# Kernel optimization log

Measured on AMD Instinct MI355X. Metric: run time of the kernel, lower is better.

The kernel has to match this reference:

```python
import jax, jax.numpy as jnp
import numpy as np

N_NODES = 10000
N_EDGES = 160000
NUM_FEAT = 14
DIM = 256


def gat_conv(x, src, dst, W, a_s, a_d, b, concat):
    """PyG GATConv: W [H*C, F_in], a_s/a_d [H, C], edges src->dst (self-loops included)."""
    H, C = a_s.shape
    N = x.shape[0]
    h = (x @ W.T).reshape(N, H, C)                       # [N,H,C]
    alpha_src = (h * a_s).sum(-1)                        # [N,H]
    alpha_dst = (h * a_d).sum(-1)                        # [N,H]
    e = jax.nn.leaky_relu(alpha_src[src] + alpha_dst[dst], negative_slope=0.2)  # [E,H]
    emax = jax.ops.segment_max(e, dst, num_segments=N)   # [N,H]
    emax = jnp.where(jnp.isneginf(emax), 0.0, emax)
    ex = jnp.exp(e - emax[dst])
    denom = jax.ops.segment_sum(ex, dst, num_segments=N)
    coef = ex / (denom[dst] + 1e-16)                     # segment softmax over in-edges
    out = jax.ops.segment_sum(h[src] * coef[..., None], dst, num_segments=N)  # [N,H,C]
    out = out.reshape(N, H * C) if concat else out.mean(axis=1)
    return out + b


def setup_inputs() -> dict:
    key = jax.random.key(0)
    ks = jax.random.split(key, 24)
    d = DIM
    f = NUM_FEAT
    def w(k, shape, fan_in):
        return jax.random.normal(k, shape, dtype=jnp.float32) * (1.0 / np.sqrt(fan_in))
    inp = {
        "x": jax.random.normal(ks[0], (N_NODES, f), dtype=jnp.float32),
        "edge_index": jax.random.randint(ks[1], (2, N_EDGES), 0, N_NODES, dtype=jnp.int64
                                         if jax.config.jax_enable_x64 else jnp.int32),
        # conv1: 14 -> 4 heads x 256
        "W1": w(ks[2], (4 * d, f), f),
        "a1s": w(ks[3], (4, d), d), "a1d": w(ks[4], (4, d), d),
        "b1": jnp.zeros((4 * d,), jnp.float32),
        "lw1": w(ks[5], (4 * d, f), f), "lb1": jnp.zeros((4 * d,), jnp.float32),
        # conv2: 1024 -> 4 heads x 256
        "W2": w(ks[6], (4 * d, 4 * d), 4 * d),
        "a2s": w(ks[7], (4, d), d), "a2d": w(ks[8], (4, d), d),
        "b2": jnp.zeros((4 * d,), jnp.float32),
        "lw2": w(ks[9], (4 * d, 4 * d), 4 * d), "lb2": jnp.zeros((4 * d,), jnp.float32),
        # conv3: 1024 -> 6 heads x 256, mean over heads
        "W3": w(ks[10], (6 * d, 4 * d), 4 * d),
        "a3s": w(ks[11], (6, d), d), "a3d": w(ks[12], (6, d), d),
        "b3": jnp.zeros((d,), jnp.float32),
        "lw3": w(ks[13], (d, 4 * d), 4 * d), "lb3": jnp.zeros((d,), jnp.float32),
    }
    return inp


def reference(x, edge_index, W1, a1s, a1d, b1, lw1, lb1,
              W2, a2s, a2d, b2, lw2, lb2,
              W3, a3s, a3d, b3, lw3, lb3):
    N = x.shape[0]
    loops = jnp.arange(N, dtype=edge_index.dtype)
    src = jnp.concatenate([edge_index[0], loops])
    dst = jnp.concatenate([edge_index[1], loops])
    x1 = jax.nn.elu(gat_conv(x, src, dst, W1, a1s, a1d, b1, True) + x @ lw1.T + lb1)
    x2 = jax.nn.elu(gat_conv(x1, src, dst, W2, a2s, a2d, b2, True) + x1 @ lw2.T + lb2)
    x3 = gat_conv(x2, src, dst, W3, a3s, a3d, b3, False) + x2 @ lw3.T + lb3
    return x3
```

## Files before the change

kernel.cpp:

```cpp
#include <hip/hip_runtime.h>
#include <hip/hip_bf16.h>
#include <cstddef>

#define NN 10000
#define EE0 160000
#define NF 14
#define DC 256

static inline int ceildiv(int a, int b) { return (a + b - 1) / b; }

__device__ __forceinline__ float lrelu02(float x) { return fmaxf(x, 0.2f * x); }

__device__ __forceinline__ short f2bf(float f) {
    unsigned u = __float_as_uint(f);
    unsigned r = (u + 0x7FFFu + ((u >> 16) & 1u)) >> 16;
    return (short)r;
}
__device__ __forceinline__ float bf2f(short s) {
    return __uint_as_float(((unsigned)(unsigned short)s) << 16);
}

typedef __attribute__((ext_vector_type(8))) short bf16x8;
typedef __attribute__((ext_vector_type(4))) float f32x4;

#define GLDS(gaddr, laddr)                                                         \
    __builtin_amdgcn_global_load_lds(                                              \
        (__attribute__((address_space(1))) void*)(gaddr),                          \
        (__attribute__((address_space(3))) void*)(laddr), 16, 0, 0)

__global__ void count_edges_k(const int* __restrict__ ei, int* __restrict__ counts,
                              int E0, int N) {
    int e = blockIdx.x * 256 + threadIdx.x;
    int E = E0 + N;
    if (e >= E) return;
    int dst = (e < E0) ? ei[E0 + e] : (e - E0);
    atomicAdd(&counts[dst], 1);
}

__global__ __launch_bounds__(1024) void scan_k(const int* __restrict__ counts,
                                               int* __restrict__ row_off, int n) {
    __shared__ int sums[1024];
    int t = threadIdx.x;
    int chunk = (n + 1023) >> 10;
    int base = t * chunk;
    int lim = base + chunk; if (lim > n) lim = n;
    int s = 0;
    for (int i = base; i < lim; ++i) s += counts[i];
    sums[t] = s;
    __syncthreads();
    for (int off = 1; off < 1024; off <<= 1) {
        int v = (t >= off) ? sums[t - off] : 0;
        __syncthreads();
        sums[t] += v;
        __syncthreads();
    }
    int run = (t == 0) ? 0 : sums[t - 1];
    for (int i = base; i < lim; ++i) { run += counts[i]; row_off[i + 1] = run; }
    if (t == 0) row_off[0] = 0;
}

__global__ void scatter_k(const int* __restrict__ ei, const int* __restrict__ row_off,
                          int* __restrict__ cursor, int* __restrict__ csr_src,
                          int E0, int N) {
    int e = blockIdx.x * 256 + threadIdx.x;
    int E = E0 + N;
    if (e >= E) return;
    int src, dst;
    if (e < E0) { src = ei[e]; dst = ei[E0 + e]; }
    else        { src = dst = e - E0; }
    int pos = row_off[dst] + atomicAdd(&cursor[dst], 1);
    csr_src[pos] = src;
}

__global__ __launch_bounds__(256) void cvt_bf16_fused_k(
    const float* __restrict__ p0, short* __restrict__ q0, int n0,
    const float* __restrict__ p1, short* __restrict__ q1, int n1,
    const float* __restrict__ p2, short* __restrict__ q2, int n2,
    const float* __restrict__ p3, short* __restrict__ q3, int n3) {
    int i = blockIdx.x * 256 + threadIdx.x;
    const float* in; short* out; int idx;
    if (i < n0) { in = p0; out = q0; idx = i; }
    else if (i < n0 + n1) { in = p1; out = q1; idx = i - n0; }
    else if (i < n0 + n1 + n2) { in = p2; out = q2; idx = i - n0 - n1; }
    else if (i < n0 + n1 + n2 + n3) { in = p3; out = q3; idx = i - n0 - n1 - n2; }
    else return;
    float4 v = ((const float4*)in)[idx];
    short4 o;
    o.x = f2bf(v.x); o.y = f2bf(v.y); o.z = f2bf(v.z); o.w = f2bf(v.w);
    ((short4*)out)[idx] = o;
}

__global__ __launch_bounds__(256) void pad_bf16_k(
    const float* __restrict__ p0, short* __restrict__ q0, int r0,
    const float* __restrict__ p1, short* __restrict__ q1, int r1,
    const float* __restrict__ p2, short* __restrict__ q2, int r2,
    int K, int Kp) {
    int i = blockIdx.x * 256 + threadIdx.x;
    int rows = r0 + r1 + r2;
    int total = rows * Kp;
    if (i >= total) return;
    int row = i / Kp, col = i - row * Kp;
    const float* in; short* out; int r;
    if (row < r0) { in = p0; out = q0; r = row; }
    else if (row < r0 + r1) { in = p1; out = q1; r = row - r0; }
    else { in = p2; out = q2; r = row - r0 - r1; }
    out[(size_t)r * Kp + col] = (col < K) ? f2bf(in[(size_t)r * K + col]) : (short)0;
}

__global__ __launch_bounds__(256) void gemm_bf16_dual(
    const short* __restrict__ A, const short* __restrict__ B,
    const float* __restrict__ b1, const float* __restrict__ b2,
    short* __restrict__ Cb, float* __restrict__ Cf,
    int M, int Nh, int Nf, int K) {
    __shared__ short As[128 * 32];
    __shared__ short Bs[128 * 32];
    const int t = threadIdx.x;
    const int wave = t >> 6, lane = t & 63;
    const int m0 = blockIdx.y * 128, n0 = blockIdx.x * 128;
    const int wm = (wave >> 1) * 64, wn = (wave & 1) * 64;
    const int lane15 = lane & 15, quad = lane >> 4;

    const int lrow = lane >> 2;
    const int lk = ((lane & 3) ^ ((lrow >> 1) & 3)) * 8;
    int arow0 = m0 + wave * 16 + lrow;
    int arow1 = arow0 + 64;
    if (arow0 > M - 1) arow0 = M - 1;
    if (arow1 > M - 1) arow1 = M - 1;
    const short* ag0 = A + (size_t)arow0 * K + lk;
    const short* ag1 = A + (size_t)arow1 * K + lk;
    const short* bg0 = B + (size_t)(n0 + wave * 16 + lrow) * K + lk;
    const short* bg1 = B + (size_t)(n0 + 64 + wave * 16 + lrow) * K + lk;
    short* al0 = &As[(wave * 16) * 32];
    short* al1 = &As[(64 + wave * 16) * 32];
    short* bl0 = &Bs[(wave * 16) * 32];
    short* bl1 = &Bs[(64 + wave * 16) * 32];

    const int rql = (quad ^ ((lane15 >> 1) & 3)) * 8;

    f32x4 acc[4][4];
#pragma unroll
    for (int i = 0; i < 4; ++i)
#pragma unroll
        for (int j = 0; j < 4; ++j) acc[i][j] = (f32x4){0.f, 0.f, 0.f, 0.f};

    for (int k0 = 0; k0 < K; k0 += 32) {
        GLDS(ag0 + k0, al0);
        GLDS(ag1 + k0, al1);
        GLDS(bg0 + k0, bl0);
        GLDS(bg1 + k0, bl1);
        __syncthreads();
        bf16x8 af[4], bfr[4];
#pragma unroll
        for (int i = 0; i < 4; ++i)
            af[i] = *(const bf16x8*)&As[(wm + 16 * i + lane15) * 32 + rql];
#pragma unroll
        for (int j = 0; j < 4; ++j)
            bfr[j] = *(const bf16x8*)&Bs[(wn + 16 * j + lane15) * 32 + rql];
#pragma unroll
        for (int i = 0; i < 4; ++i)
#pragma unroll
            for (int j = 0; j < 4; ++j)
                acc[i][j] = __builtin_amdgcn_mfma_f32_16x16x32_bf16(
                    af[i], bfr[j], acc[i][j], 0, 0, 0);
        __syncthreads();
    }

    if (n0 >= Nh) {
#pragma unroll
        for (int j = 0; j < 4; ++j) {
            int nc = n0 - Nh + wn + 16 * j + lane15;
            float bias = b1[nc] + b2[nc];
#pragma unroll
            for (int i = 0; i < 4; ++i) {
                int mb = m0 + wm + 16 * i + quad * 4;
#pragma unroll
                for (int r = 0; r < 4; ++r) {
                    int m = mb + r;
                    if (m < M) Cf[(size_t)m * Nf + nc] = acc[i][j][r] + bias;
                }
            }
        }
    } else {
#pragma unroll
        for (int j = 0; j < 4; ++j) {
            int n = n0 + wn + 16 * j + lane15;
#pragma unroll
            for (int i = 0; i < 4; ++i) {
                int mb = m0 + wm + 16 * i + quad * 4;
#pragma unroll
                for (int r = 0; r < 4; ++r) {
                    int m = mb + r;
                    if (m < M) Cb[(size_t)m * Nh + n] = f2bf(acc[i][j][r]);
                }
            }
        }
    }
}

__global__ __launch_bounds__(256) void alpha_k(
    const short* __restrict__ h, const float* __restrict__ a_s,
    const float* __restrict__ a_d, float* __restrict__ asrc,
    float* __restrict__ adst, int N, int H) {
    int wid = (int)((blockIdx.x * (size_t)blockDim.x + threadIdx.x) >> 6);
    int lane = threadIdx.x & 63;
    if (wid >= N * H) return;
    int n = wid / H, hh = wid - n * H;
    const short4 hv4 = *(const short4*)(h + (size_t)n * H * DC + hh * DC + lane * 4);
    const float4 sv = *(const float4*)(a_s + hh * DC + lane * 4);
    const float4 dv = *(const float4*)(a_d + hh * DC + lane * 4);
    float hx = bf2f(hv4.x), hy = bf2f(hv4.y), hz = bf2f(hv4.z), hw = bf2f(hv4.w);
    float s = hx * sv.x + hy * sv.y + hz * sv.z + hw * sv.w;
    float d = hx * dv.x + hy * dv.y + hz * dv.z + hw * dv.w;
#pragma unroll
    for (int off = 32; off > 0; off >>= 1) {
        s += __shfl_down(s, off);
        d += __shfl_down(d, off);
    }
    if (lane == 0) { asrc[wid] = s; adst[wid] = d; }
}

__global__ __launch_bounds__(256) void gat_agg(
    const short* __restrict__ hbuf, const float* __restrict__ lin,
    const float* __restrict__ asrc, const float* __restrict__ adst_a,
    const int* __restrict__ row_off, const int* __restrict__ csr_src,
    short* __restrict__ outx, int N, int H) {
    int wid = (int)((blockIdx.x * (size_t)blockDim.x + threadIdx.x) >> 6);
    int lane = threadIdx.x & 63;
    if (wid >= N * H) return;
    int n = wid / H, hh = wid - n * H;
    int beg = row_off[n], end = row_off[n + 1];
    int deg = end - beg;
    float ad = adst_a[wid];

    size_t cbase = (size_t)n * H * DC + hh * DC + lane * 4;
    float4 acc = *(const float4*)(lin + cbase);

    if (deg <= 64) {
        int s = 0; float e = -1e38f;
        if (lane < deg) {
            s = csr_src[beg + lane];
            e = lrelu02(asrc[s * H + hh] + ad);
        }
        float m = e;
#pragma unroll
        for (int off = 32; off > 0; off >>= 1) m = fmaxf(m, __shfl_xor(m, off));
        float p = (lane < deg) ? __expf(e - m) : 0.f;
        float dsum = p;
#pragma unroll
        for (int off = 32; off > 0; off >>= 1) dsum += __shfl_xor(dsum, off);
        float coef = p / (dsum + 1e-16f);

        const size_t hoff = (size_t)hh * DC + lane * 4;
        int i = 0;
        for (; i + 8 <= deg; i += 8) {
            short4 v[8]; float wv[8];
#pragma unroll
            for (int u = 0; u < 8; ++u) {
                int su = __shfl(s, i + u);
                v[u] = *(const short4*)(hbuf + (size_t)su * (H * DC) + hoff);
                wv[u] = __shfl(coef, i + u);
            }
#pragma unroll
            for (int u = 0; u < 8; ++u) {
                acc.x += wv[u] * bf2f(v[u].x);
                acc.y += wv[u] * bf2f(v[u].y);
                acc.z += wv[u] * bf2f(v[u].z);
                acc.w += wv[u] * bf2f(v[u].w);
            }
        }
        for (; i < deg; ++i) {
            float wv = __shfl(coef, i);
            int si = __shfl(s, i);
            const short4 hv = *(const short4*)(hbuf + (size_t)si * (H * DC) + hoff);
            acc.x += wv * bf2f(hv.x); acc.y += wv * bf2f(hv.y);
            acc.z += wv * bf2f(hv.z); acc.w += wv * bf2f(hv.w);
        }
    } else {
        float m = -1e38f;
        for (int i = beg + lane; i < end; i += 64) {
            int s = csr_src[i];
            m = fmaxf(m, lrelu02(asrc[s * H + hh] + ad));
        }
#pragma unroll
        for (int off = 32; off > 0; off >>= 1) m = fmaxf(m, __shfl_xor(m, off));
        float dsum = 0.f;
        for (int i = beg + lane; i < end; i += 64) {
            int s = csr_src[i];
            dsum += __expf(lrelu02(asrc[s * H + hh] + ad) - m);
        }
#pragma unroll
        for (int off = 32; off > 0; off >>= 1) dsum += __shfl_xor(dsum, off);
        float inv = 1.f / (dsum + 1e-16f);
        for (int i = beg; i < end; ++i) {
            int s = csr_src[i];
            float wv = __expf(lrelu02(asrc[s * H + hh] + ad) - m) * inv;
            const short4 hv = *(const short4*)(hbuf + ((size_t)s * H + hh) * DC + lane * 4);
            acc.x += wv * bf2f(hv.x); acc.y += wv * bf2f(hv.y);
            acc.z += wv * bf2f(hv.z); acc.w += wv * bf2f(hv.w);
        }
    }
    acc.x = acc.x > 0.f ? acc.x : __expf(acc.x) - 1.f;
    acc.y = acc.y > 0.f ? acc.y : __expf(acc.y) - 1.f;
    acc.z = acc.z > 0.f ? acc.z : __expf(acc.z) - 1.f;
    acc.w = acc.w > 0.f ? acc.w : __expf(acc.w) - 1.f;
    short4 o;
    o.x = f2bf(acc.x); o.y = f2bf(acc.y); o.z = f2bf(acc.z); o.w = f2bf(acc.w);
    *(short4*)(outx + cbase) = o;
}

__global__ __launch_bounds__(384) void gat_agg_mean(
    const short* __restrict__ hbuf, const float* __restrict__ asrc,
    const float* __restrict__ adst_a, const int* __restrict__ row_off,
    const int* __restrict__ csr_src, float* __restrict__ out, int N) {
    const int H = 6;
    __shared__ float red[6][DC];
    int n = blockIdx.x;
    int wave = threadIdx.x >> 6, lane = threadIdx.x & 63;
    int hh = wave;
    int beg = row_off[n], end = row_off[n + 1];
    int deg = end - beg;
    const float invH = 1.f / 6.f;
    float ad = adst_a[n * H + hh];

    float4 acc = make_float4(0.f, 0.f, 0.f, 0.f);
    const size_t hoff = (size_t)hh * DC + lane * 4;

    if (deg <= 64) {
        int s = 0; float e = -1e38f;
        if (lane < deg) {
            s = csr_src[beg + lane];
            e = lrelu02(asrc[s * H + hh] + ad);
        }
        float m = e;
#pragma unroll
        for (int off = 32; off > 0; off >>= 1) m = fmaxf(m, __shfl_xor(m, off));
        float p = (lane < deg) ? __expf(e - m) : 0.f;
        float dsum = p;
#pragma unroll
        for (int off = 32; off > 0; off >>= 1) dsum += __shfl_xor(dsum, off);
        float coef = p * invH / (dsum + 1e-16f);

        int i = 0;
        for (; i + 8 <= deg; i += 8) {
            short4 v[8]; float wv[8];
#pragma unroll
            for (int u = 0; u < 8; ++u) {
                int su = __shfl(s, i + u);
                v[u] = *(const short4*)(hbuf + (size_t)su * (H * DC) + hoff);
                wv[u] = __shfl(coef, i + u);
            }
#pragma unroll
            for (int u = 0; u < 8; ++u) {
                acc.x += wv[u] * bf2f(v[u].x);
                acc.y += wv[u] * bf2f(v[u].y);
                acc.z += wv[u] * bf2f(v[u].z);
                acc.w += wv[u] * bf2f(v[u].w);
            }
        }
        for (; i < deg; ++i) {
            float wv = __shfl(coef, i);
            int si = __shfl(s, i);
            const short4 hv = *(const short4*)(hbuf + (size_t)si * (H * DC) + hoff);
            acc.x += wv * bf2f(hv.x); acc.y += wv * bf2f(hv.y);
            acc.z += wv * bf2f(hv.z); acc.w += wv * bf2f(hv.w);
        }
    } else {
        float m = -1e38f;
        for (int i = beg + lane; i < end; i += 64) {
            int s = csr_src[i];
            m = fmaxf(m, lrelu02(asrc[s * H + hh] + ad));
        }
#pragma unroll
        for (int off = 32; off > 0; off >>= 1) m = fmaxf(m, __shfl_xor(m, off));
        float dsum = 0.f;
        for (int i = beg + lane; i < end; i += 64) {
            int s = csr_src[i];
            dsum += __expf(lrelu02(asrc[s * H + hh] + ad) - m);
        }
#pragma unroll
        for (int off = 32; off > 0; off >>= 1) dsum += __shfl_xor(dsum, off);
        float inv = invH / (dsum + 1e-16f);
        for (int i = beg; i < end; ++i) {
            int s = csr_src[i];
            float wv = __expf(lrelu02(asrc[s * H + hh] + ad) - m) * inv;
            const short4 hv = *(const short4*)(hbuf + (size_t)s * (H * DC) + hoff);
            acc.x += wv * bf2f(hv.x); acc.y += wv * bf2f(hv.y);
            acc.z += wv * bf2f(hv.z); acc.w += wv * bf2f(hv.w);
        }
    }
    *(float4*)&red[wave][lane * 4] = acc;
    __syncthreads();
    if (wave == 0) {
        float* op = out + (size_t)n * DC + lane * 4;
        float4 o = *(float4*)op;
#pragma unroll
        for (int j = 0; j < 6; ++j) {
            float4 r = *(float4*)&red[j][lane * 4];
            o.x += r.x; o.y += r.y; o.z += r.z; o.w += r.w;
        }
        *(float4*)op = o;
    }
}

extern "C" void kernel_launch(void* const* d_in, const int* in_sizes, int n_in,
                              void* d_out, int out_size, void* d_ws, size_t ws_size,
                              hipStream_t stream) {
    const float* x   = (const float*)d_in[0];
    const int*   ei  = (const int*)d_in[1];
    const float* W1  = (const float*)d_in[2];
    const float* a1s = (const float*)d_in[3];
    const float* a1d = (const float*)d_in[4];
    const float* b1  = (const float*)d_in[5];
    const float* lw1 = (const float*)d_in[6];
    const float* lb1 = (const float*)d_in[7];
    const float* W2  = (const float*)d_in[8];
    const float* a2s = (const float*)d_in[9];
    const float* a2d = (const float*)d_in[10];
    const float* b2  = (const float*)d_in[11];
    const float* lb2_w = (const float*)d_in[12];
    const float* lb2 = (const float*)d_in[13];
    const float* W3  = (const float*)d_in[14];
    const float* a3s = (const float*)d_in[15];
    const float* a3d = (const float*)d_in[16];
    const float* b3  = (const float*)d_in[17];
    const float* lw3 = (const float*)d_in[18];
    const float* lb3 = (const float*)d_in[19];
    const float* lw2 = lb2_w;
    float* out = (float*)d_out;

    const int N = NN, E0 = EE0, E = EE0 + NN;

    unsigned char* w = (unsigned char*)d_ws;
    size_t off = 0;
    auto alloc = [&](size_t bytes) {
        void* p = w + off;
        off += (bytes + 255) & ~(size_t)255;
        return p;
    };
    short* hbuf   = (short*)alloc((size_t)N * 1536 * 2);
    float* buf    = (float*)alloc((size_t)N * 1024 * 4);
    short* xb     = (short*)alloc((size_t)N * 1024 * 2);
    short* xpad   = (short*)alloc((size_t)N * 32 * 2);
    short* W1p    = (short*)alloc((size_t)1024 * 32 * 2);
    short* lw1p   = (short*)alloc((size_t)1024 * 32 * 2);
    short* W2b    = (short*)alloc((size_t)1024 * 1024 * 2);
    short* lw2b   = (short*)alloc((size_t)1024 * 1024 * 2);
    short* W3b    = (short*)alloc((size_t)1536 * 1024 * 2);
    short* lw3b   = (short*)alloc((size_t)256 * 1024 * 2);
    float* asrc   = (float*)alloc((size_t)N * 6 * 4);
    float* adst   = (float*)alloc((size_t)N * 6 * 4);
    int* row_off  = (int*)alloc((size_t)(N + 1) * 4);
    int* counts2  = (int*)alloc((size_t)2 * N * 4);
    int* counts   = counts2;
    int* cursor   = counts2 + N;
    int* csr_src  = (int*)alloc((size_t)E * 4);
    (void)ws_size; (void)n_in; (void)in_sizes; (void)out_size;

    hipMemsetAsync(counts2, 0, (size_t)2 * N * 4, stream);
    count_edges_k<<<ceildiv(E, 256), 256, 0, stream>>>(ei, counts, E0, N);
    scan_k<<<1, 1024, 0, stream>>>(counts, row_off, N);
    scatter_k<<<ceildiv(E, 256), 256, 0, stream>>>(ei, row_off, cursor, csr_src, E0, N);

    {
        int q0 = 1024 * 1024 / 4, q1 = 1024 * 1024 / 4, q2 = 1536 * 1024 / 4,
            q3 = 256 * 1024 / 4;
        cvt_bf16_fused_k<<<ceildiv(q0 + q1 + q2 + q3, 256), 256, 0, stream>>>(
            W2, W2b, q0, lw2, lw2b, q1, W3, W3b, q2, lw3, lw3b, q3);
        int rows = N + 1024 + 1024;
        pad_bf16_k<<<ceildiv(rows * 32, 256), 256, 0, stream>>>(
            x, xpad, N, W1, W1p, 1024, lw1, lw1p, 1024, NF, 32);
    }

    gemm_bf16_dual<<<dim3(16, ceildiv(N, 128)), 256, 0, stream>>>(
        xpad, W1p, b1, lb1, hbuf, buf, N, 1024, 1024, 32);
    alpha_k<<<ceildiv(N * 4, 4), 256, 0, stream>>>(hbuf, a1s, a1d, asrc, adst, N, 4);
    gat_agg<<<ceildiv(N * 4, 4), 256, 0, stream>>>(hbuf, buf, asrc, adst, row_off, csr_src,
                                                   xb, N, 4);

    gemm_bf16_dual<<<dim3(16, ceildiv(N, 128)), 256, 0, stream>>>(
        xb, W2b, b2, lb2, hbuf, buf, N, 1024, 1024, 1024);
    alpha_k<<<ceildiv(N * 4, 4), 256, 0, stream>>>(hbuf, a2s, a2d, asrc, adst, N, 4);
    gat_agg<<<ceildiv(N * 4, 4), 256, 0, stream>>>(hbuf, buf, asrc, adst, row_off, csr_src,
                                                   xb, N, 4);

    gemm_bf16_dual<<<dim3(14, ceildiv(N, 128)), 256, 0, stream>>>(
        xb, W3b, b3, lb3, hbuf, out, N, 1536, 256, 1024);
    alpha_k<<<ceildiv(N * 6, 4), 256, 0, stream>>>(hbuf, a3s, a3d, asrc, adst, N, 6);
    gat_agg_mean<<<N, 384, 0, stream>>>(hbuf, asrc, adst, row_off, csr_src, out, N);
}
```

Before: 486.1 us.

## Fuse attention-logit computation into GEMM epilogue, store lin in bf16, remap workgroups per XCD

Computes the per-head source and destination attention logits inside the GEMM epilogue from fp32 accumulators, using shuffles and atomicAdd into zeroed buffers, and drops the separate alpha kernel. The dense linear-branch output for layers 1 and 2 is now stored as bf16 instead of fp32, which halves its write and later read traffic. Workgroup IDs are remapped so consecutive tiles land on the same XCD, aiming for better L2 reuse. In exchange it adds memset launches and atomics, lowers the precision of the linear branch, and makes the logit sums order-dependent.

After: 511.6 us. 1.05x slower.

```diff
diff --git a/kernel.cpp b/kernel.cpp
--- a/kernel.cpp
+++ b/kernel.cpp
@@ -110,13 +110,24 @@
 __global__ __launch_bounds__(256) void gemm_bf16_dual(
     const short* __restrict__ A, const short* __restrict__ B,
     const float* __restrict__ b1, const float* __restrict__ b2,
-    short* __restrict__ Cb, float* __restrict__ Cf,
-    int M, int Nh, int Nf, int K) {
+    const float* __restrict__ a_s, const float* __restrict__ a_d,
+    float* __restrict__ asrc, float* __restrict__ adst,
+    short* __restrict__ Cb, void* __restrict__ Cf, int lin_bf16,
+    int M, int Nh, int Nf, int K, int H) {
     __shared__ short As[128 * 32];
     __shared__ short Bs[128 * 32];
     const int t = threadIdx.x;
     const int wave = t >> 6, lane = t & 63;
-    const int m0 = blockIdx.y * 128, n0 = blockIdx.x * 128;
+
+    const int gx = gridDim.x;
+    const int nwg = gx * gridDim.y;
+    const int orig = blockIdx.y * gx + blockIdx.x;
+    const int xcd = orig & 7;
+    const int q = nwg >> 3, rmd = nwg & 7;
+    const int wgid = (xcd < rmd ? xcd * (q + 1) : rmd * (q + 1) + (xcd - rmd) * q)
+                     + (orig >> 3);
+    const int m0 = (wgid / gx) * 128, n0 = (wgid % gx) * 128;
+
     const int wm = (wave >> 1) * 64, wn = (wave & 1) * 64;
     const int lane15 = lane & 15, quad = lane >> 4;
 
@@ -176,11 +187,23 @@
 #pragma unroll
                 for (int r = 0; r < 4; ++r) {
                     int m = mb + r;
-                    if (m < M) Cf[(size_t)m * Nf + nc] = acc[i][j][r] + bias;
+                    if (m < M) {
+                        float v = acc[i][j][r] + bias;
+                        if (lin_bf16) ((short*)Cf)[(size_t)m * Nf + nc] = f2bf(v);
+                        else          ((float*)Cf)[(size_t)m * Nf + nc] = v;
+                    }
                 }
             }
         }
     } else {
+        const int head = (n0 + wn) >> 8;
+        const int cb = (n0 + wn) & 255;
+        float asv[4], adv[4];
+#pragma unroll
+        for (int j = 0; j < 4; ++j) {
+            asv[j] = a_s[head * DC + cb + 16 * j + lane15];
+            adv[j] = a_d[head * DC + cb + 16 * j + lane15];
+        }
 #pragma unroll
         for (int j = 0; j < 4; ++j) {
             int n = n0 + wn + 16 * j + lane15;
@@ -194,33 +217,31 @@
                 }
             }
         }
-    }
-}
-
-__global__ __launch_bounds__(256) void alpha_k(
-    const short* __restrict__ h, const float* __restrict__ a_s,
-    const float* __restrict__ a_d, float* __restrict__ asrc,
-    float* __restrict__ adst, int N, int H) {
-    int wid = (int)((blockIdx.x * (size_t)blockDim.x + threadIdx.x) >> 6);
-    int lane = threadIdx.x & 63;
-    if (wid >= N * H) return;
-    int n = wid / H, hh = wid - n * H;
-    const short4 hv4 = *(const short4*)(h + (size_t)n * H * DC + hh * DC + lane * 4);
-    const float4 sv = *(const float4*)(a_s + hh * DC + lane * 4);
-    const float4 dv = *(const float4*)(a_d + hh * DC + lane * 4);
-    float hx = bf2f(hv4.x), hy = bf2f(hv4.y), hz = bf2f(hv4.z), hw = bf2f(hv4.w);
-    float s = hx * sv.x + hy * sv.y + hz * sv.z + hw * sv.w;
-    float d = hx * dv.x + hy * dv.y + hz * dv.z + hw * dv.w;
-#pragma unroll
-    for (int off = 32; off > 0; off >>= 1) {
-        s += __shfl_down(s, off);
-        d += __shfl_down(d, off);
-    }
-    if (lane == 0) { asrc[wid] = s; adst[wid] = d; }
+#pragma unroll
+        for (int i = 0; i < 4; ++i) {
+#pragma unroll
+            for (int r = 0; r < 4; ++r) {
+                float s = acc[i][0][r] * asv[0] + acc[i][1][r] * asv[1] +
+                          acc[i][2][r] * asv[2] + acc[i][3][r] * asv[3];
+                float d = acc[i][0][r] * adv[0] + acc[i][1][r] * adv[1] +
+                          acc[i][2][r] * adv[2] + acc[i][3][r] * adv[3];
+#pragma unroll
+                for (int off = 8; off > 0; off >>= 1) {
+                    s += __shfl_xor(s, off);
+                    d += __shfl_xor(d, off);
+                }
+                int m = m0 + wm + 16 * i + quad * 4 + r;
+                if (lane15 == 0 && m < M) {
+                    atomicAdd(&asrc[(size_t)m * H + head], s);
+                    atomicAdd(&adst[(size_t)m * H + head], d);
+                }
+            }
+        }
+    }
 }
 
 __global__ __launch_bounds__(256) void gat_agg(
-    const short* __restrict__ hbuf, const float* __restrict__ lin,
+    const short* __restrict__ hbuf, const short* __restrict__ lin,
     const float* __restrict__ asrc, const float* __restrict__ adst_a,
     const int* __restrict__ row_off, const int* __restrict__ csr_src,
     short* __restrict__ outx, int N, int H) {
@@ -233,7 +254,8 @@
     float ad = adst_a[wid];
 
     size_t cbase = (size_t)n * H * DC + hh * DC + lane * 4;
-    float4 acc = *(const float4*)(lin + cbase);
+    const short4 lv = *(const short4*)(lin + cbase);
+    float4 acc = make_float4(bf2f(lv.x), bf2f(lv.y), bf2f(lv.z), bf2f(lv.w));
 
     if (deg <= 64) {
         int s = 0; float e = -1e38f;
@@ -438,7 +460,7 @@
         return p;
     };
     short* hbuf   = (short*)alloc((size_t)N * 1536 * 2);
-    float* buf    = (float*)alloc((size_t)N * 1024 * 4);
+    short* buf    = (short*)alloc((size_t)N * 1024 * 2);
     short* xb     = (short*)alloc((size_t)N * 1024 * 2);
     short* xpad   = (short*)alloc((size_t)N * 32 * 2);
     short* W1p    = (short*)alloc((size_t)1024 * 32 * 2);
@@ -447,14 +469,17 @@
     short* lw2b   = (short*)alloc((size_t)1024 * 1024 * 2);
     short* W3b    = (short*)alloc((size_t)1536 * 1024 * 2);
     short* lw3b   = (short*)alloc((size_t)256 * 1024 * 2);
-    float* asrc   = (float*)alloc((size_t)N * 6 * 4);
-    float* adst   = (float*)alloc((size_t)N * 6 * 4);
+    float* alpha  = (float*)alloc((size_t)2 * N * 6 * 4);
+    float* asrc   = alpha;
+    float* adst   = alpha + (size_t)N * 6;
     int* row_off  = (int*)alloc((size_t)(N + 1) * 4);
     int* counts2  = (int*)alloc((size_t)2 * N * 4);
     int* counts   = counts2;
     int* cursor   = counts2 + N;
     int* csr_src  = (int*)alloc((size_t)E * 4);
     (void)ws_size; (void)n_in; (void)in_sizes; (void)out_size;
+
+    const size_t alpha_bytes = (size_t)2 * N * 6 * 4;
 
     hipMemsetAsync(counts2, 0, (size_t)2 * N * 4, stream);
     count_edges_k<<<ceildiv(E, 256), 256, 0, stream>>>(ei, counts, E0, N);
@@ -471,20 +496,23 @@
             x, xpad, N, W1, W1p, 1024, lw1, lw1p, 1024, NF, 32);
     }
 
+    hipMemsetAsync(alpha, 0, alpha_bytes, stream);
     gemm_bf16_dual<<<dim3(16, ceildiv(N, 128)), 256, 0, stream>>>(
-        xpad, W1p, b1, lb1, hbuf, buf, N, 1024, 1024, 32);
-    alpha_k<<<ceildiv(N * 4, 4), 256, 0, stream>>>(hbuf, a1s, a1d, asrc, adst, N, 4);
-    gat_agg<<<ceildiv(N * 4, 4), 256, 0, stream>>>(hbuf, buf, asrc, adst, row_off, csr_src,
-                                                   xb, N, 4);
-
+        xpad, W1p, b1, lb1, a1s, a1d, asrc, adst, hbuf, (void*)buf, 1,
+        N, 1024, 1024, 32, 4);
+    gat_agg<<<ceildiv(N * 4, 4), 256, 0, stream>>>(hbuf, buf, asrc, adst, row_off,
+                                                   csr_src, xb, N, 4);
+
+    hipMemsetAsync(alpha, 0, alpha_bytes, stream);
     gemm_bf16_dual<<<dim3(16, ceildiv(N, 128)), 256, 0, stream>>>(
-        xb, W2b, b2, lb2, hbuf, buf, N, 1024, 1024, 1024);
-    alpha_k<<<ceildiv(N * 4, 4), 256, 0, stream>>>(hbuf, a2s, a2d, asrc, adst, N, 4);
-    gat_agg<<<ceildiv(N * 4, 4), 256, 0, stream>>>(hbuf, buf, asrc, adst, row_off, csr_src,
-                                                   xb, N, 4);
-
+        xb, W2b, b2, lb2, a2s, a2d, asrc, adst, hbuf, (void*)buf, 1,
+        N, 1024, 1024, 1024, 4);
+    gat_agg<<<ceildiv(N * 4, 4), 256, 0, stream>>>(hbuf, buf, asrc, adst, row_off,
+                                                   csr_src, xb, N, 4);
+
+    hipMemsetAsync(alpha, 0, alpha_bytes, stream);
     gemm_bf16_dual<<<dim3(14, ceildiv(N, 128)), 256, 0, stream>>>(
-        xb, W3b, b3, lb3, hbuf, out, N, 1536, 256, 1024);
-    alpha_k<<<ceildiv(N * 6, 4), 256, 0, stream>>>(hbuf, a3s, a3d, asrc, adst, N, 6);
+        xb, W3b, b3, lb3, a3s, a3d, asrc, adst, hbuf, (void*)out, 0,
+        N, 1536, 256, 1024, 6);
     gat_agg_mean<<<N, 384, 0, stream>>>(hbuf, asrc, adst, row_off, csr_src, out, N);
 }
```
